# Performance work log

Hardware: AMD Instinct MI355X
Metric: run time of the kernel (lower is better)

## Reference

```python
import jax, jax.numpy as jnp
import numpy as np

EPS = 1e-8      # torch F.cosine_similarity eps
MARGIN = 0.6
POS_MASK = 2.0  # added at the positive location before top-k mining
K_NEG = 4


def setup_inputs() -> dict:
    key = jax.random.key(0)
    k1, k2, k3, k4 = jax.random.split(key, 4)
    B, C, H, W = 4, 256, 64, 64
    sketch = jax.random.normal(k1, (B, C, H, W), dtype=jnp.float32)
    ref = jax.random.normal(k2, (B, C, H, W), dtype=jnp.float32)
    # one anchor coordinate per positive grid cell (B*H*W pairs total)
    anchor_y = jax.random.randint(k3, (B, H * W), 0, H, dtype=jnp.int32)
    anchor_x = jax.random.randint(k4, (B, H * W), 0, W, dtype=jnp.int32)
    return {"sketch_query_vectors": sketch, "ref_key_vectors": ref,
            "anchor_y": anchor_y, "anchor_x": anchor_x}


def reference(sketch_query_vectors, ref_key_vectors, anchor_y, anchor_x):
    B, C, H, W = sketch_query_vectors.shape
    M = H * W  # ref locations; also number of positive pairs per batch elem

    sketch_flat = sketch_query_vectors.reshape(B, C, M)  # (B, C, M)
    ref_flat = ref_key_vectors.reshape(B, C, M)          # (B, C, M)

    # gather anchor features at (anchor_y, anchor_x): flat index ay*W + ax
    a_idx = anchor_y * W + anchor_x                      # (B, N), N == M
    anchors = jnp.take_along_axis(sketch_flat, a_idx[:, None, :], axis=2)  # (B, C, N)
    anchors = anchors.transpose(0, 2, 1)                 # (B, N, C)

    # cosine similarity of each anchor vs full ref map of same batch elem
    dot = jnp.einsum('bnc,bcm->bnm', anchors, ref_flat)  # (B, N, M)
    a_norm = jnp.linalg.norm(anchors, axis=-1)           # (B, N)
    r_norm = jnp.linalg.norm(ref_flat, axis=1)           # (B, M)
    sim = dot / jnp.maximum(a_norm[:, :, None] * r_norm[:, None, :], EPS)
    dist = 1.0 - sim                                     # (B, N, M)

    # positive location for pair n is grid cell n -> diagonal
    pos_distance = jnp.mean(jnp.diagonal(dist, axis1=1, axis2=2))

    # mask the positive location then mine 4 smallest distances
    masked = dist + POS_MASK * jnp.eye(M, dtype=dist.dtype)[None, :, :]
    neg_vals = -jax.lax.top_k(-masked, K_NEG)[0]         # (B, N, K_NEG)
    neg_loss = jnp.mean(jnp.maximum(MARGIN - neg_vals, 0.0))

    return pos_distance + neg_loss
```

## Files before the change

kernel.cpp:

```cpp
#include <hip/hip_runtime.h>
#include <math.h>

#define B_  4
#define C_  256
#define W_  64
#define M_  4096
#define N_  4096
#define THRESH_ 0.4f

typedef __attribute__((ext_vector_type(8))) short bf16x8;
typedef __attribute__((ext_vector_type(4))) float f32x4;

__device__ __forceinline__ short f2bf(float x) {
    union { float f; unsigned u; } v; v.f = x;
    unsigned r = v.u + 0x7fffu + ((v.u >> 16) & 1u);
    return (short)(r >> 16);
}
__device__ __forceinline__ float bf2f(short s) {
    union { unsigned u; float f; } v;
    v.u = ((unsigned)(unsigned short)s) << 16;
    return v.f;
}
__device__ __forceinline__ void gload_lds16(const void* g, void* l) {
    __builtin_amdgcn_global_load_lds(
        (const __attribute__((address_space(1))) void*)g,
        (__attribute__((address_space(3))) void*)l, 16, 0, 0);
}

#define OFF_ANCH   0
#define OFF_REFT   8388608
#define OFF_IA     16777216
#define OFF_IR     16842752
#define OFF_DIAG   16908288
#define OFF_SSUM   16973824
#define OFF_ROWSUM 17235968
#define OFF_ROWCNT 17301504
#define OFF_FLAGC  17367040
#define OFF_FLAGL  17367296

__global__ __launch_bounds__(256) void gather_kernel(
    const float* __restrict__ sketch,
    const int* __restrict__ ay, const int* __restrict__ ax,
    short* __restrict__ anchors, float* __restrict__ ia)
{
    const int pair = blockIdx.x;
    const int b = pair >> 12;
    const int c = threadIdx.x;
    const int idx = ay[pair] * W_ + ax[pair];
    const float v = sketch[((size_t)(b * C_ + c)) * M_ + idx];
    anchors[(size_t)pair * C_ + c] = f2bf(v);

    __shared__ float red[256];
    red[c] = v * v;
    __syncthreads();
    for (int s = 128; s > 0; s >>= 1) {
        if (c < s) red[c] += red[c + s];
        __syncthreads();
    }
    if (c == 0) ia[pair] = rsqrtf(red[0]);
}

__global__ __launch_bounds__(256) void convert_kernel(
    const float* __restrict__ ref, short* __restrict__ refT,
    float* __restrict__ ssum)
{
    const int bx = blockIdx.x;
    const int cq = blockIdx.y;
    const int b  = bx >> 4;
    const int m  = (bx & 15) * 256 + threadIdx.x;

    const float* src = ref + ((size_t)(b * C_ + cq * 64)) * M_ + m;
    short* dst = refT + ((size_t)(b * M_ + m)) * C_ + cq * 64;

    float ss = 0.f;
#pragma unroll
    for (int j8 = 0; j8 < 8; ++j8) {
        bf16x8 v;
#pragma unroll
        for (int e = 0; e < 8; ++e) {
            float x = src[(size_t)(j8 * 8 + e) * M_];
            ss += x * x;
            v[e] = f2bf(x);
        }
        *reinterpret_cast<bf16x8*>(dst + j8 * 8) = v;
    }
    ssum[(size_t)cq * (B_ * M_) + b * M_ + m] = ss;
}

__global__ __launch_bounds__(256) void rnorm_fin_kernel(
    const float* __restrict__ ssum, float* __restrict__ ir)
{
    const int i = blockIdx.x * 256 + threadIdx.x;
    float s = ssum[i] + ssum[B_ * M_ + i] + ssum[2 * B_ * M_ + i]
            + ssum[3 * B_ * M_ + i];
    ir[i] = rsqrtf(s);
}

#define BK 64

__global__ __launch_bounds__(256) void gemm_kernel(
    const short* __restrict__ anchors, const short* __restrict__ refT,
    const float* __restrict__ ia, const float* __restrict__ ir,
    float* __restrict__ diag, float* __restrict__ rowsum,
    int* __restrict__ rowcnt)
{
    const int mBase = blockIdx.x * 128;
    const int nBase = blockIdx.y * 128;
    const int b = blockIdx.z;
    const int tid = threadIdx.x;
    const int lane = tid & 63, wv = tid >> 6;
    const int wm = (wv >> 1) * 64, wn = (wv & 1) * 64;
    const int l15 = lane & 15, l4 = lane >> 4;

    __shared__ __align__(16) short Rs[128 * BK];
    __shared__ __align__(16) short As[128 * BK];

    const short* refT_b = refT + ((size_t)b * M_ + mBase) * C_;
    const short* anch_b = anchors + ((size_t)b * N_ + nBase) * C_;

    f32x4 acc[4][4] = {};

    for (int k0 = 0; k0 < C_; k0 += BK) {
#pragma unroll
        for (int c = 0; c < 4; ++c) {
            const int cb = wv * 4 + c;
            const int row = cb * 8 + (lane >> 3);
            const int kk = (lane & 7) * 8;
            gload_lds16(refT_b + (size_t)row * C_ + k0 + kk, (char*)Rs + cb * 1024);
            gload_lds16(anch_b + (size_t)row * C_ + k0 + kk, (char*)As + cb * 1024);
        }
        __syncthreads();

#pragma unroll
        for (int ks = 0; ks < 2; ++ks) {
            bf16x8 pm[4], pn[4];
#pragma unroll
            for (int f = 0; f < 4; ++f) {
                pm[f] = *reinterpret_cast<const bf16x8*>(
                    &Rs[(wm + f * 16 + l15) * BK + ks * 32 + l4 * 8]);
                pn[f] = *reinterpret_cast<const bf16x8*>(
                    &As[(wn + f * 16 + l15) * BK + ks * 32 + l4 * 8]);
            }
#pragma unroll
            for (int fi = 0; fi < 4; ++fi)
#pragma unroll
                for (int fj = 0; fj < 4; ++fj)
                    acc[fi][fj] = __builtin_amdgcn_mfma_f32_16x16x32_bf16(
                        pm[fi], pn[fj], acc[fi][fj], 0, 0, 0);
        }
        __syncthreads();
    }

    float irv[4][4];
#pragma unroll
    for (int fi = 0; fi < 4; ++fi)
#pragma unroll
        for (int r = 0; r < 4; ++r)
            irv[fi][r] = ir[b * M_ + mBase + wm + fi * 16 + l4 * 4 + r];

#pragma unroll
    for (int fj = 0; fj < 4; ++fj) {
        const int gn = nBase + wn + fj * 16 + l15;
        const float ian = ia[b * N_ + gn];
        float s = 0.f; int cnt = 0;
#pragma unroll
        for (int fi = 0; fi < 4; ++fi) {
#pragma unroll
            for (int r = 0; r < 4; ++r) {
                const int gm = mBase + wm + fi * 16 + l4 * 4 + r;
                const float sim = acc[fi][fj][r] * irv[fi][r] * ian;
                if (gm == gn) {
                    diag[b * N_ + gn] = 1.0f - sim;
                } else if (sim > THRESH_) {
                    s += sim - THRESH_; ++cnt;
                }
            }
        }
        if (cnt) {
            atomicAdd(&rowsum[b * N_ + gn], s);
            atomicAdd(&rowcnt[b * N_ + gn], cnt);
        }
    }
}

__global__ __launch_bounds__(256) void flag_kernel(
    const int* __restrict__ rowcnt, int* __restrict__ flagcnt,
    int* __restrict__ flaglist)
{
    int i = blockIdx.x * 256 + threadIdx.x;
    if (rowcnt[i] > 4) {
        int p = atomicAdd(flagcnt, 1);
        flaglist[p] = i;
    }
}

__global__ __launch_bounds__(256) void fallback_kernel(
    const short* __restrict__ anchors, const short* __restrict__ refT,
    const float* __restrict__ ia, const float* __restrict__ ir,
    const int* __restrict__ flagcnt, const int* __restrict__ flaglist,
    float* __restrict__ rowsum)
{
    const int nflag = *flagcnt;
    __shared__ float av[C_];
    __shared__ float tops[256][4];
    for (int fi = blockIdx.x; fi < nflag; fi += gridDim.x) {
        const int row = flaglist[fi];
        const int b = row >> 12, n = row & (N_ - 1);
        __syncthreads();
        av[threadIdx.x] = bf2f(anchors[(size_t)row * C_ + threadIdx.x]);
        __syncthreads();
        const float ian = ia[row];
        float t0 = 0, t1 = 0, t2 = 0, t3 = 0;
        for (int m = threadIdx.x; m < M_; m += 256) {
            if (m == n) continue;
            const short* rp = refT + ((size_t)b * M_ + m) * C_;
            float dot = 0.f;
#pragma unroll 8
            for (int c = 0; c < C_; ++c) dot += av[c] * bf2f(rp[c]);
            float rl = dot * ian * ir[b * M_ + m] - THRESH_;
            if (rl > t3) {
                t3 = rl;
                if (t3 > t2) { float t = t2; t2 = t3; t3 = t; }
                if (t2 > t1) { float t = t1; t1 = t2; t2 = t; }
                if (t1 > t0) { float t = t0; t0 = t1; t1 = t; }
            }
        }
        tops[threadIdx.x][0] = t0; tops[threadIdx.x][1] = t1;
        tops[threadIdx.x][2] = t2; tops[threadIdx.x][3] = t3;
        __syncthreads();
        if (threadIdx.x == 0) {
            float s0 = 0, s1 = 0, s2 = 0, s3 = 0;
            for (int t = 0; t < 1024; ++t) {
                float v = tops[t >> 2][t & 3];
                if (v > s3) {
                    s3 = v;
                    if (s3 > s2) { float tt = s2; s2 = s3; s3 = tt; }
                    if (s2 > s1) { float tt = s1; s1 = s2; s2 = tt; }
                    if (s1 > s0) { float tt = s0; s0 = s1; s1 = tt; }
                }
            }
            rowsum[row] = s0 + s1 + s2 + s3;
        }
        __syncthreads();
    }
}

__global__ __launch_bounds__(256) void final_kernel(
    const float* __restrict__ rowsum, const float* __restrict__ diag,
    float* __restrict__ out)
{
    float sn = 0.f, sp = 0.f;
    for (int i = threadIdx.x; i < B_ * N_; i += 256) {
        sn += rowsum[i];
        sp += diag[i];
    }
    __shared__ float red[256];
    red[threadIdx.x] = sp * (1.0f / (B_ * N_)) + sn * (1.0f / (B_ * N_ * 4));
    __syncthreads();
    for (int s = 128; s > 0; s >>= 1) {
        if (threadIdx.x < s) red[threadIdx.x] += red[threadIdx.x + s];
        __syncthreads();
    }
    if (threadIdx.x == 0) out[0] = red[0];
}

extern "C" void kernel_launch(void* const* d_in, const int* in_sizes, int n_in,
                              void* d_out, int out_size, void* d_ws, size_t ws_size,
                              hipStream_t stream)
{
    const float* sketch = (const float*)d_in[0];
    const float* ref    = (const float*)d_in[1];
    const int*   ay     = (const int*)d_in[2];
    const int*   ax     = (const int*)d_in[3];
    float* out = (float*)d_out;

    char* ws = (char*)d_ws;
    short* anchors  = (short*)(ws + OFF_ANCH);
    short* refT     = (short*)(ws + OFF_REFT);
    float* ia       = (float*)(ws + OFF_IA);
    float* ir       = (float*)(ws + OFF_IR);
    float* diag     = (float*)(ws + OFF_DIAG);
    float* ssum     = (float*)(ws + OFF_SSUM);
    float* rowsum   = (float*)(ws + OFF_ROWSUM);
    int*   rowcnt   = (int*)(ws + OFF_ROWCNT);
    int*   flagcnt  = (int*)(ws + OFF_FLAGC);
    int*   flaglist = (int*)(ws + OFF_FLAGL);

    hipMemsetAsync(ws + OFF_ROWSUM, 0, OFF_FLAGL - OFF_ROWSUM, stream);

    gather_kernel<<<B_ * N_, 256, 0, stream>>>(sketch, ay, ax, anchors, ia);
    convert_kernel<<<dim3(64, 4), 256, 0, stream>>>(ref, refT, ssum);
    rnorm_fin_kernel<<<(B_ * M_) / 256, 256, 0, stream>>>(ssum, ir);

    gemm_kernel<<<dim3(M_ / 128, N_ / 128, B_), 256, 0, stream>>>(
        anchors, refT, ia, ir, diag, rowsum, rowcnt);

    flag_kernel<<<(B_ * N_) / 256, 256, 0, stream>>>(rowcnt, flagcnt, flaglist);
    fallback_kernel<<<64, 256, 0, stream>>>(anchors, refT, ia, ir,
                                            flagcnt, flaglist, rowsum);
    final_kernel<<<1, 256, 0, stream>>>(rowsum, diag, out);
}
```

Measured before the change: 176.1 us.

## Transpose whole sketch to bf16 and gather anchors inside GEMM with swizzled LDS

Drops the per-pair gather kernel and instead converts the full sketch tensor to a channel-last bf16 layout in the same launch as the ref conversion. The GEMM reads anchor rows indirectly through a precomputed flat index, and anchor norms are looked up from per-location sketch norms. It also adds an XOR swizzle to the LDS tile layout to reduce bank conflicts on the fragment reads, and replaces the memset with a small init kernel that also computes the anchor indices. The cost is converting the whole sketch rather than only the gathered rows, plus indirect row addressing in the GEMM. The workspace is rearranged so the enlarged norm scratch buffer overlaps later buffers, which relies on the launch order.

After: 156.3 us. 1.13x faster.

```diff
diff --git a/kernel.cpp b/kernel.cpp
--- a/kernel.cpp
+++ b/kernel.cpp
@@ -27,50 +27,30 @@
         (__attribute__((address_space(3))) void*)l, 16, 0, 0);
 }
 
-#define OFF_ANCH   0
+#define OFF_SKT    0
 #define OFF_REFT   8388608
-#define OFF_IA     16777216
+#define OFF_ISN    16777216
 #define OFF_IR     16842752
+#define OFF_SSUM   16908288
 #define OFF_DIAG   16908288
-#define OFF_SSUM   16973824
-#define OFF_ROWSUM 17235968
-#define OFF_ROWCNT 17301504
-#define OFF_FLAGC  17367040
-#define OFF_FLAGL  17367296
-
-__global__ __launch_bounds__(256) void gather_kernel(
-    const float* __restrict__ sketch,
-    const int* __restrict__ ay, const int* __restrict__ ax,
-    short* __restrict__ anchors, float* __restrict__ ia)
-{
-    const int pair = blockIdx.x;
-    const int b = pair >> 12;
-    const int c = threadIdx.x;
-    const int idx = ay[pair] * W_ + ax[pair];
-    const float v = sketch[((size_t)(b * C_ + c)) * M_ + idx];
-    anchors[(size_t)pair * C_ + c] = f2bf(v);
-
-    __shared__ float red[256];
-    red[c] = v * v;
-    __syncthreads();
-    for (int s = 128; s > 0; s >>= 1) {
-        if (c < s) red[c] += red[c + s];
-        __syncthreads();
-    }
-    if (c == 0) ia[pair] = rsqrtf(red[0]);
-}
+#define OFF_ROWSUM 16973824
+#define OFF_ROWCNT 17039360
+#define OFF_FLAGC  17104896
+#define OFF_FLAGL  17105152
+#define OFF_AIDX   17170688
 
 __global__ __launch_bounds__(256) void convert_kernel(
-    const float* __restrict__ ref, short* __restrict__ refT,
+    const float* __restrict__ sketch, const float* __restrict__ ref,
+    short* __restrict__ sketchT, short* __restrict__ refT,
     float* __restrict__ ssum)
 {
-    const int bx = blockIdx.x;
+    const int b  = blockIdx.x >> 4;
+    const int m  = (blockIdx.x & 15) * 256 + threadIdx.x;
     const int cq = blockIdx.y;
-    const int b  = bx >> 4;
-    const int m  = (bx & 15) * 256 + threadIdx.x;
-
-    const float* src = ref + ((size_t)(b * C_ + cq * 64)) * M_ + m;
-    short* dst = refT + ((size_t)(b * M_ + m)) * C_ + cq * 64;
+    const int z  = blockIdx.z;
+
+    const float* src = (z ? ref : sketch) + ((size_t)(b * C_ + cq * 64)) * M_ + m;
+    short* dst = (z ? refT : sketchT) + ((size_t)(b * M_ + m)) * C_ + cq * 64;
 
     float ss = 0.f;
 #pragma unroll
@@ -84,23 +64,42 @@
         }
         *reinterpret_cast<bf16x8*>(dst + j8 * 8) = v;
     }
-    ssum[(size_t)cq * (B_ * M_) + b * M_ + m] = ss;
-}
-
-__global__ __launch_bounds__(256) void rnorm_fin_kernel(
-    const float* __restrict__ ssum, float* __restrict__ ir)
+    ssum[(size_t)(z * 4 + cq) * (B_ * M_) + b * M_ + m] = ss;
+}
+
+__global__ __launch_bounds__(256) void fin_kernel(
+    const float* __restrict__ ssum, float* __restrict__ isn,
+    float* __restrict__ ir)
 {
     const int i = blockIdx.x * 256 + threadIdx.x;
-    float s = ssum[i] + ssum[B_ * M_ + i] + ssum[2 * B_ * M_ + i]
-            + ssum[3 * B_ * M_ + i];
-    ir[i] = rsqrtf(s);
+    float s0 = 0.f, s1 = 0.f;
+#pragma unroll
+    for (int cq = 0; cq < 4; ++cq) {
+        s0 += ssum[(size_t)cq * (B_ * M_) + i];
+        s1 += ssum[(size_t)(4 + cq) * (B_ * M_) + i];
+    }
+    isn[i] = rsqrtf(s0);
+    ir[i]  = rsqrtf(s1);
+}
+
+__global__ __launch_bounds__(256) void prep2_kernel(
+    const int* __restrict__ ay, const int* __restrict__ ax,
+    int* __restrict__ aidx, float* __restrict__ rowsum,
+    int* __restrict__ rowcnt, int* __restrict__ flagcnt)
+{
+    const int i = blockIdx.x * 256 + threadIdx.x;
+    aidx[i] = ay[i] * W_ + ax[i];
+    rowsum[i] = 0.f;
+    rowcnt[i] = 0;
+    if (i == 0) *flagcnt = 0;
 }
 
 #define BK 64
 
 __global__ __launch_bounds__(256) void gemm_kernel(
-    const short* __restrict__ anchors, const short* __restrict__ refT,
-    const float* __restrict__ ia, const float* __restrict__ ir,
+    const short* __restrict__ sketchT, const short* __restrict__ refT,
+    const int* __restrict__ aidx,
+    const float* __restrict__ isn, const float* __restrict__ ir,
     float* __restrict__ diag, float* __restrict__ rowsum,
     int* __restrict__ rowcnt)
 {
@@ -111,12 +110,21 @@
     const int lane = tid & 63, wv = tid >> 6;
     const int wm = (wv >> 1) * 64, wn = (wv & 1) * 64;
     const int l15 = lane & 15, l4 = lane >> 4;
+    const int l7 = lane & 7, l8 = lane >> 3;
+    const int ksw = ((l7 ^ l8) << 3);
 
     __shared__ __align__(16) short Rs[128 * BK];
     __shared__ __align__(16) short As[128 * BK];
 
-    const short* refT_b = refT + ((size_t)b * M_ + mBase) * C_;
-    const short* anch_b = anchors + ((size_t)b * N_ + nBase) * C_;
+    const short* asrc[4];
+    const short* bsrc[4];
+#pragma unroll
+    for (int c = 0; c < 4; ++c) {
+        const int row = (wv * 4 + c) * 8 + l8;
+        asrc[c] = refT + ((size_t)b * M_ + mBase + row) * C_ + ksw;
+        const int an = aidx[b * N_ + nBase + row];
+        bsrc[c] = sketchT + ((size_t)b * M_ + an) * C_ + ksw;
+    }
 
     f32x4 acc[4][4] = {};
 
@@ -124,10 +132,8 @@
 #pragma unroll
         for (int c = 0; c < 4; ++c) {
             const int cb = wv * 4 + c;
-            const int row = cb * 8 + (lane >> 3);
-            const int kk = (lane & 7) * 8;
-            gload_lds16(refT_b + (size_t)row * C_ + k0 + kk, (char*)Rs + cb * 1024);
-            gload_lds16(anch_b + (size_t)row * C_ + k0 + kk, (char*)As + cb * 1024);
+            gload_lds16(asrc[c] + k0, (char*)Rs + cb * 1024);
+            gload_lds16(bsrc[c] + k0, (char*)As + cb * 1024);
         }
         __syncthreads();
 
@@ -136,10 +142,11 @@
             bf16x8 pm[4], pn[4];
 #pragma unroll
             for (int f = 0; f < 4; ++f) {
-                pm[f] = *reinterpret_cast<const bf16x8*>(
-                    &Rs[(wm + f * 16 + l15) * BK + ks * 32 + l4 * 8]);
-                pn[f] = *reinterpret_cast<const bf16x8*>(
-                    &As[(wn + f * 16 + l15) * BK + ks * 32 + l4 * 8]);
+                const int rowA = wm + f * 16 + l15;
+                const int rowB = wn + f * 16 + l15;
+                const int kphys = ((ks * 4 + l4) ^ (l15 & 7)) << 3;
+                pm[f] = *reinterpret_cast<const bf16x8*>(&Rs[rowA * BK + kphys]);
+                pn[f] = *reinterpret_cast<const bf16x8*>(&As[rowB * BK + kphys]);
             }
 #pragma unroll
             for (int fi = 0; fi < 4; ++fi)
@@ -161,7 +168,7 @@
 #pragma unroll
     for (int fj = 0; fj < 4; ++fj) {
         const int gn = nBase + wn + fj * 16 + l15;
-        const float ian = ia[b * N_ + gn];
+        const float ian = isn[b * M_ + aidx[b * N_ + gn]];
         float s = 0.f; int cnt = 0;
 #pragma unroll
         for (int fi = 0; fi < 4; ++fi) {
@@ -195,8 +202,9 @@
 }
 
 __global__ __launch_bounds__(256) void fallback_kernel(
-    const short* __restrict__ anchors, const short* __restrict__ refT,
-    const float* __restrict__ ia, const float* __restrict__ ir,
+    const short* __restrict__ sketchT, const short* __restrict__ refT,
+    const int* __restrict__ aidx,
+    const float* __restrict__ isn, const float* __restrict__ ir,
     const int* __restrict__ flagcnt, const int* __restrict__ flaglist,
     float* __restrict__ rowsum)
 {
@@ -206,10 +214,11 @@
     for (int fi = blockIdx.x; fi < nflag; fi += gridDim.x) {
         const int row = flaglist[fi];
         const int b = row >> 12, n = row & (N_ - 1);
-        __syncthreads();
-        av[threadIdx.x] = bf2f(anchors[(size_t)row * C_ + threadIdx.x]);
-        __syncthreads();
-        const float ian = ia[row];
+        const int an = aidx[row];
+        __syncthreads();
+        av[threadIdx.x] = bf2f(sketchT[((size_t)b * M_ + an) * C_ + threadIdx.x]);
+        __syncthreads();
+        const float ian = isn[b * M_ + an];
         float t0 = 0, t1 = 0, t2 = 0, t3 = 0;
         for (int m = threadIdx.x; m < M_; m += 256) {
             if (m == n) continue;
@@ -275,28 +284,29 @@
     float* out = (float*)d_out;
 
     char* ws = (char*)d_ws;
-    short* anchors  = (short*)(ws + OFF_ANCH);
+    short* sketchT  = (short*)(ws + OFF_SKT);
     short* refT     = (short*)(ws + OFF_REFT);
-    float* ia       = (float*)(ws + OFF_IA);
+    float* isn      = (float*)(ws + OFF_ISN);
     float* ir       = (float*)(ws + OFF_IR);
+    float* ssum     = (float*)(ws + OFF_SSUM);
     float* diag     = (float*)(ws + OFF_DIAG);
-    float* ssum     = (float*)(ws + OFF_SSUM);
     float* rowsum   = (float*)(ws + OFF_ROWSUM);
     int*   rowcnt   = (int*)(ws + OFF_ROWCNT);
     int*   flagcnt  = (int*)(ws + OFF_FLAGC);
     int*   flaglist = (int*)(ws + OFF_FLAGL);
-
-    hipMemsetAsync(ws + OFF_ROWSUM, 0, OFF_FLAGL - OFF_ROWSUM, stream);
-
-    gather_kernel<<<B_ * N_, 256, 0, stream>>>(sketch, ay, ax, anchors, ia);
-    convert_kernel<<<dim3(64, 4), 256, 0, stream>>>(ref, refT, ssum);
-    rnorm_fin_kernel<<<(B_ * M_) / 256, 256, 0, stream>>>(ssum, ir);
+    int*   aidx     = (int*)(ws + OFF_AIDX);
+
+    convert_kernel<<<dim3(16 * B_, 4, 2), 256, 0, stream>>>(
+        sketch, ref, sketchT, refT, ssum);
+    fin_kernel<<<(B_ * M_) / 256, 256, 0, stream>>>(ssum, isn, ir);
+    prep2_kernel<<<(B_ * N_) / 256, 256, 0, stream>>>(
+        ay, ax, aidx, rowsum, rowcnt, flagcnt);
 
     gemm_kernel<<<dim3(M_ / 128, N_ / 128, B_), 256, 0, stream>>>(
-        anchors, refT, ia, ir, diag, rowsum, rowcnt);
+        sketchT, refT, aidx, isn, ir, diag, rowsum, rowcnt);
 
     flag_kernel<<<(B_ * N_) / 256, 256, 0, stream>>>(rowcnt, flagcnt, flaglist);
-    fallback_kernel<<<64, 256, 0, stream>>>(anchors, refT, ia, ir,
+    fallback_kernel<<<64, 256, 0, stream>>>(sketchT, refT, aidx, isn, ir,
                                             flagcnt, flaglist, rowsum);
     final_kernel<<<1, 256, 0, stream>>>(rowsum, diag, out);
 }
```
